# Kernel tuning notes

Measured on AMD Instinct MI355X. Metric: run time of the kernel, lower is better.

## Reference

```python
import jax, jax.numpy as jnp
import numpy as np

N, E, F, HID, OUT, B, HEADS = 4096, 131072, 64, 64, 86, 16, 4


def setup_inputs() -> dict:
    key = jax.random.key(0)
    ks = jax.random.split(key, 12)
    s = 0.1
    return {
        "x": jax.random.normal(ks[0], (N, F), dtype=jnp.float32),
        "edge_index": jax.random.randint(ks[1], (2, E), 0, N),
        "edge_attr": jax.random.uniform(ks[2], (E,), dtype=jnp.float32),
        "batch": jnp.sort(jax.random.randint(ks[3], (N,), 0, B)).astype(jnp.int32),
        # GCNConv1: Linear(F -> HID, no bias) + post-aggregation bias
        "W1": jax.random.normal(ks[4], (HID, F), dtype=jnp.float32) * s,
        "b1": jnp.zeros((HID,), jnp.float32),
        # MultiheadAttention(embed_dim=HID, num_heads=4)
        "Win": jax.random.normal(ks[5], (3 * HID, HID), dtype=jnp.float32) * s,
        "b_in": jnp.zeros((3 * HID,), jnp.float32),
        "Wout": jax.random.normal(ks[6], (HID, HID), dtype=jnp.float32) * s,
        "b_out": jnp.zeros((HID,), jnp.float32),
        # GCNConv2: Linear(HID -> OUT)
        "W2": jax.random.normal(ks[7], (OUT, HID), dtype=jnp.float32) * s,
        "b2": jnp.zeros((OUT,), jnp.float32),
    }


def _gcn_layer(h, W, b, src_a, dst_a, norm, n):
    # x' = scatter_add(norm * (x W^T)[src] -> dst) + b   (PyG GCNConv)
    h = h @ W.T
    agg = jax.ops.segment_sum(norm[:, None] * h[src_a], dst_a, num_segments=n)
    return agg + b


def reference(x, edge_index, edge_attr, batch, W1, b1, Win, b_in, Wout, b_out, W2, b2):
    n = x.shape[0]
    # torch.cat([x[:, :-1], x[:, -1:].view(-1,1)], dim=1) == x (identity)
    src, dst = edge_index[0], edge_index[1]
    loop = jnp.arange(n)
    src_a = jnp.concatenate([src, loop])
    dst_a = jnp.concatenate([dst, loop])
    w_a = jnp.concatenate([edge_attr, jnp.ones((n,), x.dtype)])  # self-loops weight 1
    deg = jax.ops.segment_sum(w_a, dst_a, num_segments=n)
    dis = jnp.where(deg > 0, jax.lax.rsqrt(jnp.maximum(deg, 1e-12)), 0.0)
    norm = dis[src_a] * w_a * dis[dst_a]

    h = jax.nn.relu(_gcn_layer(x, W1, b1, src_a, dst_a, norm, n))  # [N, HID]

    # MultiheadAttention over the whole node set as one sequence (batch=1)
    qkv = h @ Win.T + b_in
    q, k, v = jnp.split(qkv, 3, axis=-1)
    dh = HID // HEADS
    to_heads = lambda t: t.reshape(n, HEADS, dh).transpose(1, 0, 2)  # [H, N, dh]
    q, k, v = to_heads(q), to_heads(k), to_heads(v)
    scores = jnp.einsum("hnd,hmd->hnm", q, k) * (1.0 / np.sqrt(dh))
    att = jax.nn.softmax(scores, axis=-1)
    o = jnp.einsum("hnm,hmd->hnd", att, v).transpose(1, 0, 2).reshape(n, HID)
    o = o @ Wout.T + b_out

    h2 = _gcn_layer(o, W2, b2, src_a, dst_a, norm, n)  # [N, OUT]

    # global_mean_pool over graph ids
    sums = jax.ops.segment_sum(h2, batch, num_segments=B)
    cnt = jax.ops.segment_sum(jnp.ones((n,), h2.dtype), batch, num_segments=B)
    return sums / jnp.maximum(cnt, 1.0)[:, None]
```

## Files before the change

### kernel.cpp

```cpp
#include <hip/hip_runtime.h>

constexpr int N = 4096, E = 131072, OUTF = 86, NB = 16, HEADS = 4, DH = 16;
constexpr int CAP = 128;
constexpr int NSPLIT = 8, KEYS = N / NSPLIT;
constexpr int PCKS = 8;

typedef __attribute__((ext_vector_type(8))) short short8;
typedef __attribute__((ext_vector_type(4))) float f32x4;

constexpr unsigned long long PK_MASK = (1ULL << 40) - 1;
constexpr float PK_SCALE = 1.0f / 16777216.0f;

constexpr size_t OFF_PCK   = 0;
constexpr size_t OFF_INV   = OFF_PCK + 16 * (size_t)N;
constexpr size_t OFF_BUFA  = OFF_INV + 16;
constexpr size_t OFF_QP    = OFF_BUFA + (size_t)N * 64;
constexpr size_t OFF_KP    = OFF_QP + (size_t)N * 32;
constexpr size_t OFF_VP    = OFF_KP + (size_t)N * 32;
constexpr size_t OFF_H2    = OFF_VP + (size_t)N * 32;
constexpr size_t OFF_EPAIR = OFF_H2 + (size_t)N * 86;
constexpr size_t OFF_NORMV = OFF_EPAIR + (size_t)2 * N * CAP;
constexpr size_t OFF_OPART = OFF_NORMV + (size_t)N * CAP;
constexpr size_t OFF_LPART = OFF_OPART + (size_t)HEADS * N * NSPLIT * 16;

__device__ inline unsigned short f2bf(float f) {
    unsigned u = __builtin_bit_cast(unsigned, f);
    u += 0x7FFFu + ((u >> 16) & 1u);
    return (unsigned short)(u >> 16);
}

__device__ inline float pk_deg(unsigned long long pk) {
    return (float)(pk & PK_MASK) * PK_SCALE;
}

__global__ __launch_bounds__(256) void d1_kernel(const float* __restrict__ x,
        const float* __restrict__ W1, const int* __restrict__ ei,
        const float* __restrict__ ea, const int* __restrict__ batch,
        const float* __restrict__ b2, float* __restrict__ ws, float* __restrict__ out) {
    __shared__ float4 Ws4[64 * 17];
    __shared__ float4 As4[16 * 17];
    __shared__ int bnd[NB + 1];
    int blk = blockIdx.x, tid = threadIdx.x;
    if (blk < 256) {
        float* bufA = ws + OFF_BUFA;
        for (int idx = tid; idx < 64 * 16; idx += 256)
            Ws4[(idx >> 4) * 17 + (idx & 15)] = ((const float4*)W1)[idx];
        {
            int r = tid >> 4, k4 = tid & 15;
            As4[r * 17 + k4] = ((const float4*)x)[(size_t)(blk * 16 + r) * 16 + k4];
        }
        __syncthreads();
        int r2 = tid & 7, cg = tid >> 3;
        float acc[2][2] = {};
#pragma unroll
        for (int k4 = 0; k4 < 16; ++k4) {
            float4 a0 = As4[r2 * 17 + k4], a1 = As4[(r2 + 8) * 17 + k4];
#pragma unroll
            for (int i = 0; i < 2; ++i) {
                float4 w = Ws4[(cg + 32 * i) * 17 + k4];
                acc[0][i] += a0.x * w.x + a0.y * w.y + a0.z * w.z + a0.w * w.w;
                acc[1][i] += a1.x * w.x + a1.y * w.y + a1.z * w.z + a1.w * w.w;
            }
        }
#pragma unroll
        for (int j = 0; j < 2; ++j)
#pragma unroll
            for (int i = 0; i < 2; ++i)
                bufA[(size_t)(blk * 16 + r2 + 8 * j) * 64 + cg + 32 * i] = acc[j][i];
    } else if (blk < 512) {
        unsigned long long* pck = (unsigned long long*)(ws + OFF_PCK);
        int2* epair = (int2*)(ws + OFF_EPAIR);
        int f = (blk - 256) * 256 + tid;
        int e0 = f, e1 = f + E / 2;
        int s0 = ei[e0], d0 = ei[E + e0];
        int s1 = ei[e1], d1 = ei[E + e1];
        float w0 = ea[e0], w1 = ea[e1];
        unsigned long long a0 = (1ULL << 40) + (unsigned long long)(unsigned)(w0 * 16777216.0f + 0.5f);
        unsigned long long a1 = (1ULL << 40) + (unsigned long long)(unsigned)(w1 * 16777216.0f + 0.5f);
        unsigned long long o0 = atomicAdd(&pck[(size_t)d0 * PCKS], a0);
        unsigned long long o1 = atomicAdd(&pck[(size_t)d1 * PCKS], a1);
        int p0 = (int)(o0 >> 40), p1 = (int)(o1 >> 40);
        if (p0 < CAP) epair[(size_t)d0 * CAP + p0] = make_int2(s0, __float_as_int(w0));
        if (p1 < CAP) epair[(size_t)d1 * CAP + p1] = make_int2(s1, __float_as_int(w1));
    } else {
        float* invcnt = ws + OFF_INV;
        if (tid <= NB) {
            int b = tid, lo = 0, hi = N;
            while (lo < hi) { int m = (lo + hi) >> 1; if (batch[m] < b) lo = m + 1; else hi = m; }
            bnd[tid] = lo;
        }
        __syncthreads();
        if (tid < NB) {
            int cnt = bnd[tid + 1] - bnd[tid];
            invcnt[tid] = cnt > 0 ? 1.0f / (float)cnt : 0.0f;
        }
        for (int idx = tid; idx < NB * OUTF; idx += 256) {
            int b = idx / OUTF;
            int cnt = bnd[b + 1] - bnd[b];
            out[idx] = cnt > 0 ? b2[idx - b * OUTF] : 0.0f;
        }
    }
}

__global__ __launch_bounds__(1024) void d23_kernel(const float* __restrict__ Win,
        const float* __restrict__ b1, const float* __restrict__ b_in,
        float* __restrict__ ws) {
    __shared__ float4 Ws4[16 * 200];
    __shared__ float  Af[16 * 68];

    const unsigned long long* pck = (const unsigned long long*)(ws + OFF_PCK);
    const int2*  epair = (const int2*)(ws + OFF_EPAIR);
    float*       normv = ws + OFF_NORMV;
    const float* bufA  = ws + OFF_BUFA;
    unsigned short* Qp = (unsigned short*)(ws + OFF_QP);
    unsigned short* Kp = (unsigned short*)(ws + OFF_KP);
    unsigned short* Vp = (unsigned short*)(ws + OFF_VP);

    const int tid = threadIdx.x, lane = tid & 63, wv = tid >> 6;
    for (int idx = tid; idx < 192 * 16; idx += 1024) {
        int c = idx >> 4, k4 = idx & 15;
        Ws4[k4 * 200 + c] = ((const float4*)Win)[idx];
    }

    const int node = blockIdx.x * 16 + wv;
    {
        const unsigned long long pkn = pck[(size_t)node * PCKS];
        const float di = rsqrtf(pk_deg(pkn) + 1.0f);
        float acc0 = (di * di) * bufA[(size_t)node * 64 + lane];
        float acc1 = 0.f, acc2 = 0.f, acc3 = 0.f;
        const int cnt = min((int)(pkn >> 40), CAP);
        const int2* pe = epair + (size_t)node * CAP;
        for (int base = 0; base < cnt; base += 64) {
            int rem = cnt - base;
            int   sl = 0;
            float nl = 0.f;
            if (lane < rem) {
                int2 e = pe[base + lane];
                sl = e.x;
                float w = __int_as_float(e.y);
                nl = rsqrtf(pk_deg(pck[(size_t)sl * PCKS]) + 1.0f) * w * di;
                normv[(size_t)node * CAP + base + lane] = nl;
            }
            int m = rem < 64 ? rem : 64;
            int j = 0;
            for (; j + 4 <= m; j += 4) {
                int   s0 = __shfl(sl, j),     s1 = __shfl(sl, j + 1);
                int   s2 = __shfl(sl, j + 2), s3 = __shfl(sl, j + 3);
                float n0 = __shfl(nl, j),     n1 = __shfl(nl, j + 1);
                float n2 = __shfl(nl, j + 2), n3 = __shfl(nl, j + 3);
                acc0 += n0 * bufA[(size_t)s0 * 64 + lane];
                acc1 += n1 * bufA[(size_t)s1 * 64 + lane];
                acc2 += n2 * bufA[(size_t)s2 * 64 + lane];
                acc3 += n3 * bufA[(size_t)s3 * 64 + lane];
            }
            for (; j < m; ++j) {
                int   s0 = __shfl(sl, j);
                float n0 = __shfl(nl, j);
                acc0 += n0 * bufA[(size_t)s0 * 64 + lane];
            }
        }
        Af[wv * 68 + lane] = fmaxf((acc0 + acc1) + (acc2 + acc3) + b1[lane], 0.0f);
    }
    __syncthreads();

    {
        const float4* Af4 = (const float4*)Af;
        float acc[3];
#pragma unroll
        for (int i = 0; i < 3; ++i) acc[i] = b_in[lane + 64 * i];
#pragma unroll
        for (int k4 = 0; k4 < 16; ++k4) {
            float4 a = Af4[wv * 17 + k4];
#pragma unroll
            for (int i = 0; i < 3; ++i) {
                float4 w = Ws4[k4 * 200 + lane + 64 * i];
                acc[i] += a.x * w.x + a.y * w.y + a.z * w.z + a.w * w.w;
            }
        }
        const int row = node;
#pragma unroll
        for (int i = 0; i < 3; ++i) {
            int c = lane + 64 * i;
            float v = acc[i];
            if (c < 64) {
                int h = c >> 4, d = c & 15;
                Qp[((size_t)h * N + row) * 16 + d] = f2bf(v * 0.25f);
            } else if (c < 128) {
                int c2 = c - 64, h = c2 >> 4, d = c2 & 15;
                Kp[((size_t)h * N + row) * 16 + d] = f2bf(v);
            } else {
                int c2 = c - 128, h = c2 >> 4, d = c2 & 15;
                Vp[((size_t)h * 16 + d) * N + row] = f2bf(v);
            }
        }
    }
}

__global__ __launch_bounds__(256) void attn_kernel(const float* __restrict__ ws_c,
        float* __restrict__ ws) {
    __shared__ __align__(16) unsigned short Plds[4 * 640];

    const unsigned short* Qp = (const unsigned short*)(ws_c + OFF_QP);
    const unsigned short* Kp = (const unsigned short*)(ws_c + OFF_KP);
    const unsigned short* Vp = (const unsigned short*)(ws_c + OFF_VP);
    float* opart = ws + OFF_OPART;
    float* lpart = ws + OFF_LPART;

    const int h  = blockIdx.y;
    const int sp = blockIdx.z;
    const int k0 = sp * KEYS;
    const int tid = threadIdx.x;
    const int lane = tid & 63, wv = tid >> 6;
    const int q15 = lane & 15, quad = lane >> 4;

    const int qbase = blockIdx.x * 64 + wv * 16;
    short8 qf = {};
    if (quad < 2)
        qf = *(const short8*)&Qp[((size_t)h * N + qbase + q15) * 16 + quad * 8];

    f32x4 O = {0.f, 0.f, 0.f, 0.f};
    float l = 0.f;
    unsigned short* Pw = &Plds[wv * 640];
    const unsigned short* Kh = Kp + (size_t)h * N * 16;
    const unsigned short* Vh = Vp + ((size_t)h * 16 + q15) * N + k0;

#pragma unroll 2
    for (int ch = 0; ch < KEYS / 32; ++ch) {
#pragma unroll
        for (int t = 0; t < 2; ++t) {
            short8 kf = {};
            if (quad < 2)
                kf = *(const short8*)&Kh[(size_t)(k0 + ch * 32 + t * 16 + q15) * 16 + quad * 8];
            f32x4 zero = {0.f, 0.f, 0.f, 0.f};
            f32x4 s = __builtin_amdgcn_mfma_f32_16x16x32_bf16(kf, qf, zero, 0, 0, 0);
            float p0 = __expf(s[0]), p1 = __expf(s[1]), p2 = __expf(s[2]), p3 = __expf(s[3]);
            l += p0 + p1 + p2 + p3;
            ushort4 pu;
            pu.x = f2bf(p0); pu.y = f2bf(p1); pu.z = f2bf(p2); pu.w = f2bf(p3);
            *(ushort4*)&Pw[q15 * 40 + t * 16 + quad * 4] = pu;
        }
        asm volatile("s_waitcnt lgkmcnt(0)" ::: "memory");
        short8 pf = *(const short8*)&Pw[q15 * 40 + quad * 8];
        short8 vf = *(const short8*)&Vh[ch * 32 + quad * 8];
        O = __builtin_amdgcn_mfma_f32_16x16x32_bf16(pf, vf, O, 0, 0, 0);
    }

    l += __shfl_xor(l, 16);
    l += __shfl_xor(l, 32);
    if (lane < 16)
        lpart[((size_t)h * N + qbase + q15) * NSPLIT + sp] = l;
#pragma unroll
    for (int r = 0; r < 4; ++r) {
        int query = qbase + quad * 4 + r;
        opart[(((size_t)h * N + query) * NSPLIT + sp) * 16 + q15] = O[r];
    }
}

__global__ __launch_bounds__(256) void d4b_kernel(const float* __restrict__ Wout,
        const float* __restrict__ b_out, const float* __restrict__ W2,
        float* __restrict__ ws) {
    __shared__ float4 WoS[64 * 17];
    __shared__ float4 W2S[96 * 17];
    __shared__ float  o_sh[16 * 68];
    __shared__ float  Bf[16 * 68];

    const float* opart = ws + OFF_OPART;
    const float* lpart = ws + OFF_LPART;
    float* h2pre = ws + OFF_H2;

    const int tid = threadIdx.x, qbase = blockIdx.x * 16;
    for (int idx = tid; idx < 64 * 16; idx += 256)
        WoS[(idx >> 4) * 17 + (idx & 15)] = ((const float4*)Wout)[idx];
    for (int idx = tid; idx < 86 * 16; idx += 256)
        W2S[(idx >> 4) * 17 + (idx & 15)] = ((const float4*)W2)[idx];

    for (int idx = tid; idx < 16 * 64; idx += 256) {
        int r = idx >> 6, f = idx & 63;
        int h = f >> 4, d = f & 15;
        size_t base = ((size_t)h * N + qbase + r) * NSPLIT;
        float L = 0.f, acc = 0.f;
#pragma unroll
        for (int s = 0; s < NSPLIT; ++s) {
            L += lpart[base + s];
            acc += opart[(base + s) * 16 + d];
        }
        o_sh[r * 68 + f] = acc / L;
    }
    __syncthreads();
    {
        int r = tid & 15, c0 = tid >> 4;
        float4* o4 = (float4*)o_sh;
#pragma unroll
        for (int i = 0; i < 4; ++i) {
            int c = c0 + 16 * i;
            float acc = b_out[c];
#pragma unroll
            for (int k4 = 0; k4 < 16; ++k4) {
                float4 a = o4[r * 17 + k4];
                float4 w = WoS[c * 17 + k4];
                acc += a.x * w.x + a.y * w.y + a.z * w.z + a.w * w.w;
            }
            Bf[r * 68 + c] = acc;
        }
    }
    __syncthreads();
    {
        int r = tid & 15, c0 = tid >> 4;
        float4* B4 = (float4*)Bf;
#pragma unroll
        for (int i = 0; i < 6; ++i) {
            int c = c0 + 16 * i;
            if (c < OUTF) {
                float acc = 0.f;
#pragma unroll
                for (int k4 = 0; k4 < 16; ++k4) {
                    float4 a = B4[r * 17 + k4];
                    float4 w = W2S[c * 17 + k4];
                    acc += a.x * w.x + a.y * w.y + a.z * w.z + a.w * w.w;
                }
                h2pre[(size_t)(qbase + r) * OUTF + c] = acc;
            }
        }
    }
}

__global__ __launch_bounds__(1024) void d5_kernel(const int* __restrict__ batch,
        float* __restrict__ ws, float* __restrict__ out) {
    __shared__ float vec[16][88];
    __shared__ int   bix[16];

    const unsigned long long* pck = (const unsigned long long*)(ws + OFF_PCK);
    const int2*  epair = (const int2*)(ws + OFF_EPAIR);
    const float* normv = ws + OFF_NORMV;
    const float* invcnt= ws + OFF_INV;
    const float* h2pre = ws + OFF_H2;

    const int tid = threadIdx.x;
    const int lane = tid & 63, wv = tid >> 6;
    const int node = blockIdx.x * 16 + wv;
    const bool hi2 = lane < (OUTF - 64);
    const int b = batch[node];
    const float inv = invcnt[b];
    const unsigned long long pkn = pck[(size_t)node * PCKS];
    const float di2 = 1.0f / (pk_deg(pkn) + 1.0f);
    const float* Hn = h2pre + (size_t)node * OUTF;
    float a0 = di2 * Hn[lane],                  a1 = 0.f, a2 = 0.f, a3 = 0.f;
    float c0 = hi2 ? di2 * Hn[64 + lane] : 0.f, c1 = 0.f, c2 = 0.f, c3 = 0.f;
    const int cnt = min((int)(pkn >> 40), CAP);
    const int2* pe = epair + (size_t)node * CAP;

    for (int base = 0; base < cnt; base += 64) {
        int rem = cnt - base;
        int   sl = 0;
        float nl = 0.f;
        if (lane < rem) {
            sl = pe[base + lane].x;
            nl = normv[(size_t)node * CAP + base + lane];
        }
        int m = rem < 64 ? rem : 64;
        int j = 0;
        for (; j + 4 <= m; j += 4) {
            int   s0 = __shfl(sl, j),     s1 = __shfl(sl, j + 1);
            int   s2 = __shfl(sl, j + 2), s3 = __shfl(sl, j + 3);
            float n0 = __shfl(nl, j),     n1 = __shfl(nl, j + 1);
            float n2 = __shfl(nl, j + 2), n3 = __shfl(nl, j + 3);
            const float* H0 = h2pre + (size_t)s0 * OUTF;
            const float* H1 = h2pre + (size_t)s1 * OUTF;
            const float* H2 = h2pre + (size_t)s2 * OUTF;
            const float* H3 = h2pre + (size_t)s3 * OUTF;
            a0 += n0 * H0[lane]; if (hi2) c0 += n0 * H0[64 + lane];
            a1 += n1 * H1[lane]; if (hi2) c1 += n1 * H1[64 + lane];
            a2 += n2 * H2[lane]; if (hi2) c2 += n2 * H2[64 + lane];
            a3 += n3 * H3[lane]; if (hi2) c3 += n3 * H3[64 + lane];
        }
        for (; j < m; ++j) {
            int   s0 = __shfl(sl, j);
            float n0 = __shfl(nl, j);
            const float* H0 = h2pre + (size_t)s0 * OUTF;
            a0 += n0 * H0[lane];
            if (hi2) c0 += n0 * H0[64 + lane];
        }
    }
    vec[wv][lane] = ((a0 + a1) + (a2 + a3)) * inv;
    if (hi2) vec[wv][64 + lane] = ((c0 + c1) + (c2 + c3)) * inv;
    if (lane == 0) bix[wv] = b;
    __syncthreads();
    if (tid < OUTF) {
        int curb = bix[0];
        float acc = 0.f;
#pragma unroll
        for (int w = 0; w < 16; ++w) {
            int bw = bix[w];
            if (bw != curb) {
                atomicAdd(&out[curb * OUTF + tid], acc);
                curb = bw; acc = 0.f;
            }
            acc += vec[w][tid];
        }
        atomicAdd(&out[curb * OUTF + tid], acc);
    }
}

extern "C" void kernel_launch(void* const* d_in, const int* in_sizes, int n_in,
                              void* d_out, int out_size, void* d_ws, size_t ws_size,
                              hipStream_t stream) {
    const float* x     = (const float*)d_in[0];
    const int*   ei    = (const int*)  d_in[1];
    const float* ea    = (const float*)d_in[2];
    const int*   batch = (const int*)  d_in[3];
    const float* W1    = (const float*)d_in[4];
    const float* b1    = (const float*)d_in[5];
    const float* Win   = (const float*)d_in[6];
    const float* b_in  = (const float*)d_in[7];
    const float* Wout  = (const float*)d_in[8];
    const float* b_out = (const float*)d_in[9];
    const float* W2    = (const float*)d_in[10];
    const float* b2    = (const float*)d_in[11];
    float* out = (float*)d_out;
    float* ws  = (float*)d_ws;

    hipMemsetAsync(ws + OFF_PCK, 0, (size_t)N * 64, stream);
    d1_kernel<<<513, 256, 0, stream>>>(x, W1, ei, ea, batch, b2, ws, out);
    d23_kernel<<<N / 16, 1024, 0, stream>>>(Win, b1, b_in, ws);
    attn_kernel<<<dim3(N / 64, HEADS, NSPLIT), 256, 0, stream>>>(ws, ws);
    d4b_kernel<<<N / 16, 256, 0, stream>>>(Wout, b_out, W2, ws);
    d5_kernel<<<N / 16, 1024, 0, stream>>>(batch, ws, out);
}
```

Before: 154.0 us.

## Fold second GCN layer and mean pool into per-graph weighted node sums

Since the second GCN aggregation and the mean pool are both linear, the code now precomputes a per-graph coefficient for every source node (Wc[b][node]) with atomics in d23. The attention output is then reduced by these weights before the Wout and W2 projections are applied, which happens once per graph in a small d6 kernel. This removes the per-node h2 projection, the h2pre buffer, the normv buffer and the second edge-gather pass. The edge-binning blocks are also reworked so each thread handles four edges. In exchange it adds scattered float atomics on a 16×N weight array, a larger memset, and a serial 16-block final reduction whose float summation order differs from before.

```diff
diff --git a/kernel.cpp b/kernel.cpp
--- a/kernel.cpp
+++ b/kernel.cpp
@@ -12,16 +12,16 @@
 constexpr float PK_SCALE = 1.0f / 16777216.0f;
 
 constexpr size_t OFF_PCK   = 0;
-constexpr size_t OFF_INV   = OFF_PCK + 16 * (size_t)N;
+constexpr size_t OFF_WC    = OFF_PCK + 16 * (size_t)N;
+constexpr size_t OFF_INV   = OFF_WC + 16 * (size_t)N;
 constexpr size_t OFF_BUFA  = OFF_INV + 16;
 constexpr size_t OFF_QP    = OFF_BUFA + (size_t)N * 64;
 constexpr size_t OFF_KP    = OFF_QP + (size_t)N * 32;
 constexpr size_t OFF_VP    = OFF_KP + (size_t)N * 32;
-constexpr size_t OFF_H2    = OFF_VP + (size_t)N * 32;
-constexpr size_t OFF_EPAIR = OFF_H2 + (size_t)N * 86;
-constexpr size_t OFF_NORMV = OFF_EPAIR + (size_t)2 * N * CAP;
-constexpr size_t OFF_OPART = OFF_NORMV + (size_t)N * CAP;
+constexpr size_t OFF_EPAIR = OFF_VP + (size_t)N * 32;
+constexpr size_t OFF_OPART = OFF_EPAIR + (size_t)2 * N * CAP;
 constexpr size_t OFF_LPART = OFF_OPART + (size_t)HEADS * N * NSPLIT * 16;
+constexpr size_t OFF_UPART = OFF_LPART + (size_t)HEADS * N * NSPLIT;
 
 __device__ inline unsigned short f2bf(float f) {
     unsigned u = __builtin_bit_cast(unsigned, f);
@@ -36,7 +36,7 @@
 __global__ __launch_bounds__(256) void d1_kernel(const float* __restrict__ x,
         const float* __restrict__ W1, const int* __restrict__ ei,
         const float* __restrict__ ea, const int* __restrict__ batch,
-        const float* __restrict__ b2, float* __restrict__ ws, float* __restrict__ out) {
+        float* __restrict__ ws) {
     __shared__ float4 Ws4[64 * 17];
     __shared__ float4 As4[16 * 17];
     __shared__ int bnd[NB + 1];
@@ -67,21 +67,26 @@
 #pragma unroll
             for (int i = 0; i < 2; ++i)
                 bufA[(size_t)(blk * 16 + r2 + 8 * j) * 64 + cg + 32 * i] = acc[j][i];
-    } else if (blk < 512) {
+    } else if (blk < 384) {
         unsigned long long* pck = (unsigned long long*)(ws + OFF_PCK);
         int2* epair = (int2*)(ws + OFF_EPAIR);
         int f = (blk - 256) * 256 + tid;
-        int e0 = f, e1 = f + E / 2;
-        int s0 = ei[e0], d0 = ei[E + e0];
-        int s1 = ei[e1], d1 = ei[E + e1];
-        float w0 = ea[e0], w1 = ea[e1];
-        unsigned long long a0 = (1ULL << 40) + (unsigned long long)(unsigned)(w0 * 16777216.0f + 0.5f);
-        unsigned long long a1 = (1ULL << 40) + (unsigned long long)(unsigned)(w1 * 16777216.0f + 0.5f);
-        unsigned long long o0 = atomicAdd(&pck[(size_t)d0 * PCKS], a0);
-        unsigned long long o1 = atomicAdd(&pck[(size_t)d1 * PCKS], a1);
-        int p0 = (int)(o0 >> 40), p1 = (int)(o1 >> 40);
-        if (p0 < CAP) epair[(size_t)d0 * CAP + p0] = make_int2(s0, __float_as_int(w0));
-        if (p1 < CAP) epair[(size_t)d1 * CAP + p1] = make_int2(s1, __float_as_int(w1));
+        int e[4] = { f, f + E / 4, f + E / 2, f + 3 * (E / 4) };
+        int s[4], d[4]; float w[4];
+#pragma unroll
+        for (int i = 0; i < 4; ++i) { s[i] = ei[e[i]]; d[i] = ei[E + e[i]]; w[i] = ea[e[i]]; }
+        unsigned long long o[4];
+#pragma unroll
+        for (int i = 0; i < 4; ++i) {
+            unsigned long long a = (1ULL << 40)
+                + (unsigned long long)(unsigned)(w[i] * 16777216.0f + 0.5f);
+            o[i] = atomicAdd(&pck[(size_t)d[i] * PCKS], a);
+        }
+#pragma unroll
+        for (int i = 0; i < 4; ++i) {
+            int p = (int)(o[i] >> 40);
+            if (p < CAP) epair[(size_t)d[i] * CAP + p] = make_int2(s[i], __float_as_int(w[i]));
+        }
     } else {
         float* invcnt = ws + OFF_INV;
         if (tid <= NB) {
@@ -94,23 +99,19 @@
             int cnt = bnd[tid + 1] - bnd[tid];
             invcnt[tid] = cnt > 0 ? 1.0f / (float)cnt : 0.0f;
         }
-        for (int idx = tid; idx < NB * OUTF; idx += 256) {
-            int b = idx / OUTF;
-            int cnt = bnd[b + 1] - bnd[b];
-            out[idx] = cnt > 0 ? b2[idx - b * OUTF] : 0.0f;
-        }
     }
 }
 
 __global__ __launch_bounds__(1024) void d23_kernel(const float* __restrict__ Win,
         const float* __restrict__ b1, const float* __restrict__ b_in,
-        float* __restrict__ ws) {
+        const int* __restrict__ batch, float* __restrict__ ws) {
     __shared__ float4 Ws4[16 * 200];
     __shared__ float  Af[16 * 68];
 
     const unsigned long long* pck = (const unsigned long long*)(ws + OFF_PCK);
     const int2*  epair = (const int2*)(ws + OFF_EPAIR);
-    float*       normv = ws + OFF_NORMV;
+    float*       Wc    = ws + OFF_WC;
+    const float* invcnt= ws + OFF_INV;
     const float* bufA  = ws + OFF_BUFA;
     unsigned short* Qp = (unsigned short*)(ws + OFF_QP);
     unsigned short* Kp = (unsigned short*)(ws + OFF_KP);
@@ -126,8 +127,12 @@
     {
         const unsigned long long pkn = pck[(size_t)node * PCKS];
         const float di = rsqrtf(pk_deg(pkn) + 1.0f);
+        const int bb = batch[node];
+        const float invb = invcnt[bb];
+        float* Wcb = Wc + (size_t)bb * N;
         float acc0 = (di * di) * bufA[(size_t)node * 64 + lane];
         float acc1 = 0.f, acc2 = 0.f, acc3 = 0.f;
+        if (lane == 0) atomicAdd(&Wcb[node], di * di * invb);
         const int cnt = min((int)(pkn >> 40), CAP);
         const int2* pe = epair + (size_t)node * CAP;
         for (int base = 0; base < cnt; base += 64) {
@@ -139,7 +144,7 @@
                 sl = e.x;
                 float w = __int_as_float(e.y);
                 nl = rsqrtf(pk_deg(pck[(size_t)sl * PCKS]) + 1.0f) * w * di;
-                normv[(size_t)node * CAP + base + lane] = nl;
+                atomicAdd(&Wcb[sl], nl * invb);
             }
             int m = rem < 64 ? rem : 64;
             int j = 0;
@@ -256,24 +261,16 @@
     }
 }
 
-__global__ __launch_bounds__(256) void d4b_kernel(const float* __restrict__ Wout,
-        const float* __restrict__ b_out, const float* __restrict__ W2,
-        float* __restrict__ ws) {
-    __shared__ float4 WoS[64 * 17];
-    __shared__ float4 W2S[96 * 17];
-    __shared__ float  o_sh[16 * 68];
-    __shared__ float  Bf[16 * 68];
+__global__ __launch_bounds__(256) void d4b_kernel(float* __restrict__ ws) {
+    __shared__ float o_sh[16 * 68];
+    __shared__ float Wc_sh[16][17];
 
     const float* opart = ws + OFF_OPART;
     const float* lpart = ws + OFF_LPART;
-    float* h2pre = ws + OFF_H2;
+    const float* Wc    = ws + OFF_WC;
+    float*       Upart = ws + OFF_UPART;
 
     const int tid = threadIdx.x, qbase = blockIdx.x * 16;
-    for (int idx = tid; idx < 64 * 16; idx += 256)
-        WoS[(idx >> 4) * 17 + (idx & 15)] = ((const float4*)Wout)[idx];
-    for (int idx = tid; idx < 86 * 16; idx += 256)
-        W2S[(idx >> 4) * 17 + (idx & 15)] = ((const float4*)W2)[idx];
-
     for (int idx = tid; idx < 16 * 64; idx += 256) {
         int r = idx >> 6, f = idx & 63;
         int h = f >> 4, d = f & 15;
@@ -286,118 +283,62 @@
         }
         o_sh[r * 68 + f] = acc / L;
     }
-    __syncthreads();
     {
-        int r = tid & 15, c0 = tid >> 4;
-        float4* o4 = (float4*)o_sh;
-#pragma unroll
-        for (int i = 0; i < 4; ++i) {
-            int c = c0 + 16 * i;
-            float acc = b_out[c];
-#pragma unroll
-            for (int k4 = 0; k4 < 16; ++k4) {
-                float4 a = o4[r * 17 + k4];
-                float4 w = WoS[c * 17 + k4];
-                acc += a.x * w.x + a.y * w.y + a.z * w.z + a.w * w.w;
-            }
-            Bf[r * 68 + c] = acc;
-        }
-    }
-    __syncthreads();
-    {
-        int r = tid & 15, c0 = tid >> 4;
-        float4* B4 = (float4*)Bf;
-#pragma unroll
-        for (int i = 0; i < 6; ++i) {
-            int c = c0 + 16 * i;
-            if (c < OUTF) {
-                float acc = 0.f;
-#pragma unroll
-                for (int k4 = 0; k4 < 16; ++k4) {
-                    float4 a = B4[r * 17 + k4];
-                    float4 w = W2S[c * 17 + k4];
-                    acc += a.x * w.x + a.y * w.y + a.z * w.z + a.w * w.w;
-                }
-                h2pre[(size_t)(qbase + r) * OUTF + c] = acc;
-            }
-        }
-    }
-}
-
-__global__ __launch_bounds__(1024) void d5_kernel(const int* __restrict__ batch,
-        float* __restrict__ ws, float* __restrict__ out) {
-    __shared__ float vec[16][88];
-    __shared__ int   bix[16];
-
-    const unsigned long long* pck = (const unsigned long long*)(ws + OFF_PCK);
-    const int2*  epair = (const int2*)(ws + OFF_EPAIR);
-    const float* normv = ws + OFF_NORMV;
+        int j = tid & 15, g = tid >> 4;
+        Wc_sh[j][g] = Wc[(size_t)g * N + qbase + j];
+    }
+    __syncthreads();
+    int g = tid >> 4, fq = tid & 15;
+    float4 acc = {0.f, 0.f, 0.f, 0.f};
+#pragma unroll
+    for (int j = 0; j < 16; ++j) {
+        float w = Wc_sh[j][g];
+        const float* orow = &o_sh[j * 68 + fq * 4];
+        acc.x += w * orow[0]; acc.y += w * orow[1];
+        acc.z += w * orow[2]; acc.w += w * orow[3];
+    }
+    *(float4*)&Upart[(((size_t)blockIdx.x) * 16 + g) * 64 + fq * 4] = acc;
+}
+
+__global__ __launch_bounds__(256) void d6_kernel(const float* __restrict__ Wout,
+        const float* __restrict__ b_out, const float* __restrict__ W2,
+        const float* __restrict__ b2, const float* __restrict__ ws,
+        float* __restrict__ out) {
+    __shared__ float red[4][64];
+    __shared__ float s_red[4];
+    __shared__ float U_sh[64], V_sh[64];
+
+    const float* Upart = ws + OFF_UPART;
+    const float* Wc    = ws + OFF_WC;
     const float* invcnt= ws + OFF_INV;
-    const float* h2pre = ws + OFF_H2;
-
-    const int tid = threadIdx.x;
-    const int lane = tid & 63, wv = tid >> 6;
-    const int node = blockIdx.x * 16 + wv;
-    const bool hi2 = lane < (OUTF - 64);
-    const int b = batch[node];
-    const float inv = invcnt[b];
-    const unsigned long long pkn = pck[(size_t)node * PCKS];
-    const float di2 = 1.0f / (pk_deg(pkn) + 1.0f);
-    const float* Hn = h2pre + (size_t)node * OUTF;
-    float a0 = di2 * Hn[lane],                  a1 = 0.f, a2 = 0.f, a3 = 0.f;
-    float c0 = hi2 ? di2 * Hn[64 + lane] : 0.f, c1 = 0.f, c2 = 0.f, c3 = 0.f;
-    const int cnt = min((int)(pkn >> 40), CAP);
-    const int2* pe = epair + (size_t)node * CAP;
-
-    for (int base = 0; base < cnt; base += 64) {
-        int rem = cnt - base;
-        int   sl = 0;
-        float nl = 0.f;
-        if (lane < rem) {
-            sl = pe[base + lane].x;
-            nl = normv[(size_t)node * CAP + base + lane];
-        }
-        int m = rem < 64 ? rem : 64;
-        int j = 0;
-        for (; j + 4 <= m; j += 4) {
-            int   s0 = __shfl(sl, j),     s1 = __shfl(sl, j + 1);
-            int   s2 = __shfl(sl, j + 2), s3 = __shfl(sl, j + 3);
-            float n0 = __shfl(nl, j),     n1 = __shfl(nl, j + 1);
-            float n2 = __shfl(nl, j + 2), n3 = __shfl(nl, j + 3);
-            const float* H0 = h2pre + (size_t)s0 * OUTF;
-            const float* H1 = h2pre + (size_t)s1 * OUTF;
-            const float* H2 = h2pre + (size_t)s2 * OUTF;
-            const float* H3 = h2pre + (size_t)s3 * OUTF;
-            a0 += n0 * H0[lane]; if (hi2) c0 += n0 * H0[64 + lane];
-            a1 += n1 * H1[lane]; if (hi2) c1 += n1 * H1[64 + lane];
-            a2 += n2 * H2[lane]; if (hi2) c2 += n2 * H2[64 + lane];
-            a3 += n3 * H3[lane]; if (hi2) c3 += n3 * H3[64 + lane];
-        }
-        for (; j < m; ++j) {
-            int   s0 = __shfl(sl, j);
-            float n0 = __shfl(nl, j);
-            const float* H0 = h2pre + (size_t)s0 * OUTF;
-            a0 += n0 * H0[lane];
-            if (hi2) c0 += n0 * H0[64 + lane];
-        }
-    }
-    vec[wv][lane] = ((a0 + a1) + (a2 + a3)) * inv;
-    if (hi2) vec[wv][64 + lane] = ((c0 + c1) + (c2 + c3)) * inv;
-    if (lane == 0) bix[wv] = b;
+
+    const int b = blockIdx.x, tid = threadIdx.x, lane = tid & 63, wv = tid >> 6;
+    float acc = 0.f;
+    for (int blk = wv; blk < 256; blk += 4)
+        acc += Upart[((size_t)blk * 16 + b) * 64 + lane];
+    red[wv][lane] = acc;
+    float sacc = 0.f;
+    for (int j = tid; j < N; j += 256) sacc += Wc[(size_t)b * N + j];
+#pragma unroll
+    for (int off = 1; off < 64; off <<= 1) sacc += __shfl_xor(sacc, off);
+    if (lane == 0) s_red[wv] = sacc;
+    __syncthreads();
+    if (wv == 0)
+        U_sh[lane] = (red[0][lane] + red[1][lane]) + (red[2][lane] + red[3][lane]);
+    __syncthreads();
+    const float s = (s_red[0] + s_red[1]) + (s_red[2] + s_red[3]);
+    if (tid < 64) {
+        float v = s * b_out[tid];
+#pragma unroll 8
+        for (int k = 0; k < 64; ++k) v += U_sh[k] * Wout[tid * 64 + k];
+        V_sh[tid] = v;
+    }
     __syncthreads();
     if (tid < OUTF) {
-        int curb = bix[0];
-        float acc = 0.f;
-#pragma unroll
-        for (int w = 0; w < 16; ++w) {
-            int bw = bix[w];
-            if (bw != curb) {
-                atomicAdd(&out[curb * OUTF + tid], acc);
-                curb = bw; acc = 0.f;
-            }
-            acc += vec[w][tid];
-        }
-        atomicAdd(&out[curb * OUTF + tid], acc);
+        float o = b2[tid];
+#pragma unroll 8
+        for (int f = 0; f < 64; ++f) o += V_sh[f] * W2[tid * 64 + f];
+        out[b * OUTF + tid] = invcnt[b] > 0.f ? o : 0.0f;
     }
 }
 
@@ -419,10 +360,10 @@
     float* out = (float*)d_out;
     float* ws  = (float*)d_ws;
 
-    hipMemsetAsync(ws + OFF_PCK, 0, (size_t)N * 64, stream);
-    d1_kernel<<<513, 256, 0, stream>>>(x, W1, ei, ea, batch, b2, ws, out);
-    d23_kernel<<<N / 16, 1024, 0, stream>>>(Win, b1, b_in, ws);
+    hipMemsetAsync(ws + OFF_PCK, 0, (size_t)32 * N * 4, stream);
+    d1_kernel<<<385, 256, 0, stream>>>(x, W1, ei, ea, batch, ws);
+    d23_kernel<<<N / 16, 1024, 0, stream>>>(Win, b1, b_in, batch, ws);
     attn_kernel<<<dim3(N / 64, HEADS, NSPLIT), 256, 0, stream>>>(ws, ws);
-    d4b_kernel<<<N / 16, 256, 0, stream>>>(Wout, b_out, W2, ws);
-    d5_kernel<<<N / 16, 1024, 0, stream>>>(batch, ws, out);
-}
+    d4b_kernel<<<N / 16, 256, 0, stream>>>(ws);
+    d6_kernel<<<NB, 256, 0, stream>>>(Wout, b_out, W2, b2, ws, out);
+}
```

Result: slower. 165.7 us (+7.6%).
